# Kernel optimization log

Hardware: AMD Instinct MI355X
Metric: run time of the kernel (lower is better)

## Reference

```python
import jax, jax.numpy as jnp
import numpy as np

# CUBA-LIF constants (from LavaNetwork.__init__ with beta=0.95)
THRESHOLD = 1.0
CURRENT_DECAY = 1.0   # current[t] = (1-1.0)*current[t-1] + input[t] == input[t]
VOLTAGE_DECAY = 1.0 - 0.95  # = 0.05, so v[t] = 0.95*v[t-1] + cur[t]

N_INPUT, N_HIDDEN, N_OUTPUT = 512, 2048, 4 * 64
B, T = 32, 1024


def setup_inputs() -> dict:
    key = jax.random.key(0)
    kx, k1, k2, k3, k4 = jax.random.split(key, 5)
    x = (jax.random.uniform(kx, (B, N_INPUT, T)) < 0.1).astype(jnp.float32)
    # learned params (Linear with bias); small scale so spiking is reasonable
    w1 = jax.random.normal(k1, (N_HIDDEN, N_INPUT), dtype=jnp.float32) * (1.0 / np.sqrt(N_INPUT))
    b1 = jax.random.normal(k2, (N_HIDDEN,), dtype=jnp.float32) * 0.01
    w2 = jax.random.normal(k3, (N_OUTPUT, N_HIDDEN), dtype=jnp.float32) * (1.0 / np.sqrt(N_HIDDEN))
    b2 = jax.random.normal(k4, (N_OUTPUT,), dtype=jnp.float32) * 0.01
    return {"x": x, "w1": w1, "b1": b1, "w2": w2, "b2": b2}


def _cuba_lif(cur):
    """CUBA neuron with current_decay=1 (current==synaptic input),
    leaky-integrate voltage, fire at threshold, reset voltage to 0.
    cur: (B, N, T) -> spikes (B, N, T)."""
    beta_v = 1.0 - VOLTAGE_DECAY  # 0.95

    def step(v, c_t):
        v = v * beta_v + c_t
        s = (v >= THRESHOLD).astype(v.dtype)
        v = v * (1.0 - s)  # reset-to-zero on spike (Loihi behavior)
        return v, s

    cur_t = jnp.moveaxis(cur, -1, 0)  # (T, B, N)
    v0 = jnp.zeros(cur.shape[:-1], cur.dtype)
    _, spk = jax.lax.scan(step, v0, cur_t)
    return jnp.moveaxis(spk, 0, -1)  # (B, N, T)


def reference(x, w1, b1, w2, b2):
    # layer 1: synapse (einsum 'bit,oi->bot' + bias) -> CUBA neuron
    cur1 = jnp.einsum('bit,oi->bot', x, w1) + b1[None, :, None]
    spk1 = _cuba_lif(cur1)
    # layer 2
    cur2 = jnp.einsum('bit,oi->bot', spk1, w2) + b2[None, :, None]
    spk2 = _cuba_lif(cur2)
    return (spk1, spk2)
```

## Files before the change

kernel.cpp:

```cpp
#include <hip/hip_runtime.h>


typedef int i32x4 __attribute__((ext_vector_type(4)));
typedef _Float16 f16x8 __attribute__((ext_vector_type(8)));
typedef _Float16 f16x4 __attribute__((ext_vector_type(4)));
typedef float f32x4 __attribute__((ext_vector_type(4)));

#define GLDS(g, l) __builtin_amdgcn_global_load_lds( \
    (const __attribute__((address_space(1))) void*)(g), \
    (__attribute__((address_space(3))) void*)(l), 16, 0, 0)

#define INV231 4.656612873077392578125e-10


__global__ __launch_bounds__(256) void prep_w8(const float* __restrict__ A,
                                               signed char* __restrict__ wp,
                                               int M, int K)
{
    long gt = (long)blockIdx.x * 256 + threadIdx.x;
    int kq4 = K >> 2;
    int m = (int)(gt / kq4), kq = (int)(gt % kq4);
    int k0 = kq * 4;
    int kt = k0 >> 6, kin = k0 & 63;
    int cw = ((kin >> 4) ^ (m >> 1)) & 3;
    float4 w = *(const float4*)&A[(long)m * K + k0];
    float wv[4] = {w.x, w.y, w.z, w.w};
    int pack[4] = {0, 0, 0, 0};
#pragma unroll
    for (int e = 0; e < 4; e++) {
        long k64 = (long)rint((double)wv[e] * 2147483648.0);
#pragma unroll
        for (int j = 0; j < 3; j++) {
            long r = ((k64 + 128) & 255) - 128;
            pack[j] |= ((int)r & 255) << (e * 8);
            k64 = (k64 - r) >> 8;
        }
        pack[3] |= ((int)k64 & 255) << (e * 8);
    }
#pragma unroll
    for (int p = 0; p < 4; p++)
        *(int*)&wp[(((long)kt * 4 + p) * M + m) * 64 + cw * 16 + (kin & 15)] = pack[p];
}

__global__ __launch_bounds__(256) void prep_x8(const float* __restrict__ x,
                                               unsigned char* __restrict__ xt)
{
    __shared__ float xs[64][68];
    const int b = blockIdx.z, i0 = blockIdx.y * 64, t0 = blockIdx.x * 64;
    const float* xb = x + ((long)b * 512 + i0) * 1024 + t0;
#pragma unroll
    for (int p = 0; p < 4; p++) {
        int f = threadIdx.x + p * 256;
        int i = f >> 4, t4 = (f & 15) * 4;
        *(float4*)&xs[i][t4] = *(const float4*)&xb[(long)i * 1024 + t4];
    }
    __syncthreads();
    int tt = threadIdx.x >> 2, c = threadIdx.x & 3;
    unsigned char bytes[16];
#pragma unroll
    for (int j = 0; j < 16; j++)
        bytes[j] = (unsigned char)xs[c * 16 + j][tt];
    *(uint4*)&xt[(((long)b * 8 + (i0 >> 6)) * 1024 + t0 + tt) * 64 + c * 16] =
        *(uint4*)bytes;
}

__global__ __launch_bounds__(320) void gemm_lif1(
    const signed char* __restrict__ wp,
    const unsigned char* __restrict__ act,
    const float* __restrict__ bias,
    unsigned* __restrict__ mask_ws)
{
    __shared__ signed char Ws[8][4][32][64];
    __shared__ float cs[2][256][33];

    const int b = blockIdx.x, m0 = blockIdx.y * 32;
    const int tid = threadIdx.x, lane = tid & 63, wave = tid >> 6;
    const int lm = lane & 15, lq = lane >> 4;
    const int fro = ((lq ^ (lm >> 1)) & 3) * 16;
    const unsigned char* ab = act + (long)b * 8 * 1024 * 64;

    i32x4 areg[2][4];
    double bv0 = 0.0, bv1 = 0.0;

    if (wave < 4) {
        const int gl_row = lane >> 2, gl_col = (lane & 3) * 16;
#pragma unroll
        for (int j = 0; j < 8; ++j) {
            const int r = wave + 4 * j;
            const int kt = r >> 2, p = r & 3;
            const signed char* g = wp + ((long)r * 2048 + m0 + gl_row) * 64 + gl_col;
            GLDS(g, &Ws[kt][p][0][0]);
            GLDS(g + 16 * 64, &Ws[kt][p][16][0]);
        }
        bv0 = (double)bias[m0 + lm];
        bv1 = (double)bias[m0 + 16 + lm];
#pragma unroll
        for (int f = 0; f < 4; f++)
            areg[0][f] = *(const i32x4*)
                &ab[((long)(wave * 64 + f * 16 + lm)) * 64 + lq * 16];
    }
    __syncthreads();

    double u = 0.0;
    bool sprev = false;

    for (int p = 0; p < 5; ++p) {
        if (wave < 4 && p < 4) {
            i32x4 acc[4][8];
#pragma unroll
            for (int pp = 0; pp < 4; pp++)
#pragma unroll
                for (int q = 0; q < 8; q++) acc[pp][q] = (i32x4)0;

#pragma unroll
            for (int kk = 0; kk < 8; ++kk) {
                {
                    int pn = p, kn = kk + 1;
                    if (kn == 8) { kn = 0; pn = p + 1; if (pn > 3) { pn = 3; kn = 7; } }
                    const long tt = (long)pn * 256 + wave * 64 + lm;
#pragma unroll
                    for (int f = 0; f < 4; f++)
                        areg[(kk + 1) & 1][f] = *(const i32x4*)
                            &ab[((long)kn * 1024 + tt + f * 16) * 64 + lq * 16];
                }
#pragma unroll
                for (int pp = 0; pp < 4; pp++) {
                    i32x4 w0 = *(const i32x4*)&Ws[kk][pp][lm][fro];
                    i32x4 w1 = *(const i32x4*)&Ws[kk][pp][16 + lm][fro];
#pragma unroll
                    for (int f = 0; f < 4; f++) {
                        acc[pp][f * 2 + 0] = __builtin_amdgcn_mfma_i32_16x16x64_i8(
                            areg[kk & 1][f], w0, acc[pp][f * 2 + 0], 0, 0, 0);
                        acc[pp][f * 2 + 1] = __builtin_amdgcn_mfma_i32_16x16x64_i8(
                            areg[kk & 1][f], w1, acc[pp][f * 2 + 1], 0, 0, 0);
                    }
                }
            }
            const int tb = wave * 64;
#pragma unroll
            for (int tf = 0; tf < 4; tf++)
#pragma unroll
                for (int r = 0; r < 4; r++) {
                    const int tl = tb + tf * 16 + lq * 4 + r;
#pragma unroll
                    for (int mf = 0; mf < 2; mf++) {
                        long T = acc[3][tf * 2 + mf][r];
                        T = T * 256 + acc[2][tf * 2 + mf][r];
                        T = T * 256 + acc[1][tf * 2 + mf][r];
                        T = T * 256 + acc[0][tf * 2 + mf][r];
                        cs[p & 1][tl][mf * 16 + lm] =
                            (float)((double)T * INV231 + (mf ? bv1 : bv0));
                    }
                }
        }
        if (wave == 4 && p >= 1 && lane < 32) {
            const int pp = p - 1, buf = pp & 1;
#pragma unroll 1
            for (int g = 0; g < 8; ++g) {
                unsigned mword = 0;
#pragma unroll
                for (int j = 0; j < 32; ++j) {
                    double c = (double)cs[buf][g * 32 + j][lane];
                    double a = 0.95 * u + c;
                    u = sprev ? c : a;
                    bool s = (u >= 1.0);
                    mword |= (s ? 1u : 0u) << j;
                    sprev = s;
                }
                mask_ws[((long)b * 32 + pp * 8 + g) * 2048 + m0 + lane] = mword;
            }
        }
        __syncthreads();
    }
}


__global__ __launch_bounds__(256) void expand_spk8(
    const unsigned* __restrict__ mask_ws,
    unsigned char* __restrict__ spk8)
{
    __shared__ unsigned msk[64][33];
    const int b = blockIdx.x, kt = blockIdx.y;
    const int tid = threadIdx.x;
#pragma unroll
    for (int i = 0; i < 8; ++i) {
        int idx = tid + i * 256;
        int tw = idx >> 6, m = idx & 63;
        msk[m][tw] = mask_ws[((long)b * 32 + tw) * 2048 + kt * 64 + m];
    }
    __syncthreads();
    unsigned char* dst = spk8 + ((long)b * 32 + kt) * 1024 * 64;
#pragma unroll
    for (int i = 0; i < 16; ++i) {
        int off = tid + i * 256;
        int t = off >> 2, mq = off & 3;
        int tw = t >> 5, sh = t & 31;
        unsigned w0 = 0, w1 = 0, w2 = 0, w3 = 0;
#pragma unroll
        for (int j = 0; j < 4; ++j) {
            w0 |= ((msk[mq * 16 + j][tw] >> sh) & 1u) << (8 * j);
            w1 |= ((msk[mq * 16 + 4 + j][tw] >> sh) & 1u) << (8 * j);
            w2 |= ((msk[mq * 16 + 8 + j][tw] >> sh) & 1u) << (8 * j);
            w3 |= ((msk[mq * 16 + 12 + j][tw] >> sh) & 1u) << (8 * j);
        }
        *(uint4*)&dst[(long)off * 16] = (uint4){w0, w1, w2, w3};
    }
}

__global__ __launch_bounds__(256) void expand_spk(
    const unsigned* __restrict__ mask_ws,
    float* __restrict__ spk1)
{
    __shared__ unsigned msk[8][32];
    const long rowbase = (long)blockIdx.x * 8;
    const int b = (int)(rowbase >> 11), m0 = (int)(rowbase & 2047);
    const int tid = threadIdx.x;
    {
        int w = tid >> 3, r = tid & 7;
        msk[r][w] = mask_ws[((long)b * 32 + w) * 2048 + m0 + r];
    }
    __syncthreads();
    const int r = tid >> 5, l5 = tid & 31;
    float* dst = spk1 + (rowbase + r) * 1024;
    const int sh = (l5 & 7) * 4;
#pragma unroll
    for (int j = 0; j < 8; j++) {
        const int t = l5 * 4 + j * 128;
        const unsigned w = msk[r][(l5 >> 3) + j * 4];
        float4 o;
        o.x = ((w >> sh) & 1u) ? 1.f : 0.f;
        o.y = ((w >> (sh + 1)) & 1u) ? 1.f : 0.f;
        o.z = ((w >> (sh + 2)) & 1u) ? 1.f : 0.f;
        o.w = ((w >> (sh + 3)) & 1u) ? 1.f : 0.f;
        *(float4*)&dst[t] = o;
    }
}

template <bool TRANS, int NITER, int CHUNK>
__global__ __launch_bounds__(256, 2) void gemm_i8(
    const signed char* __restrict__ wp,
    const unsigned char* __restrict__ act,
    const float* __restrict__ bias,
    float* __restrict__ C,
    int M)
{
    constexpr int NCHUNK = NITER / CHUNK;
    __shared__ signed char Ws[CHUNK][4][32][64];

    const int b = blockIdx.y;
    const int m0 = blockIdx.z * 32, t0 = blockIdx.x * 256;
    const int tid = threadIdx.x, lane = tid & 63, wave = tid >> 6;
    const int wt = t0 + wave * 64;
    const int lm = lane & 15, lq = lane >> 4;
    const int fro = ((lq ^ (lm >> 1)) & 3) * 16;
    const int gl_row = lane >> 2, gl_col = (lane & 3) * 16;

    const unsigned char* ab = act + (long)b * NITER * 1024 * 64;

    auto stage = [&](int cc) {
#pragma unroll
        for (int j = 0; j < CHUNK; ++j) {
            const int r = wave + 4 * j;
            const int kt = r >> 2, p = r & 3;
            const long kg = ((long)(cc * CHUNK + kt) * 4 + p);
            const signed char* g = wp + (kg * M + m0 + gl_row) * 64 + gl_col;
            GLDS(g, &Ws[kt][p][0][0]);
            GLDS(g + 16 * 64, &Ws[kt][p][16][0]);
        }
    };

    i32x4 acc[4][8];
#pragma unroll
    for (int p = 0; p < 4; p++)
#pragma unroll
        for (int q = 0; q < 8; q++) acc[p][q] = (i32x4)0;

    stage(0);
    i32x4 areg[2][4];
#pragma unroll
    for (int f = 0; f < 4; f++)
        areg[0][f] = *(const i32x4*)&ab[((long)(wt + f * 16 + lm)) * 64 + lq * 16];
    __syncthreads();

    for (int c = 0; c < NCHUNK; ++c) {
#pragma unroll
        for (int kk = 0; kk < CHUNK; ++kk) {
            {
                const int itv = c * CHUNK + kk;
                const long nx = (itv + 1 < NITER) ? itv + 1 : itv;
#pragma unroll
                for (int f = 0; f < 4; f++)
                    areg[(kk + 1) & 1][f] = *(const i32x4*)
                        &ab[(nx * 1024 + wt + f * 16 + lm) * 64 + lq * 16];
            }
#pragma unroll
            for (int p = 0; p < 4; p++) {
                i32x4 w0 = *(const i32x4*)&Ws[kk][p][lm][fro];
                i32x4 w1 = *(const i32x4*)&Ws[kk][p][16 + lm][fro];
                if (TRANS) {
#pragma unroll
                    for (int f = 0; f < 4; f++) {
                        acc[p][f * 2 + 0] = __builtin_amdgcn_mfma_i32_16x16x64_i8(
                            areg[kk & 1][f], w0, acc[p][f * 2 + 0], 0, 0, 0);
                        acc[p][f * 2 + 1] = __builtin_amdgcn_mfma_i32_16x16x64_i8(
                            areg[kk & 1][f], w1, acc[p][f * 2 + 1], 0, 0, 0);
                    }
                } else {
#pragma unroll
                    for (int f = 0; f < 4; f++) {
                        acc[p][0 + f] = __builtin_amdgcn_mfma_i32_16x16x64_i8(
                            w0, areg[kk & 1][f], acc[p][0 + f], 0, 0, 0);
                        acc[p][4 + f] = __builtin_amdgcn_mfma_i32_16x16x64_i8(
                            w1, areg[kk & 1][f], acc[p][4 + f], 0, 0, 0);
                    }
                }
            }
        }
        if (c + 1 < NCHUNK) {
            __syncthreads();
            stage(c + 1);
            __syncthreads();
        }
    }

    if (TRANS) {
        double bv[2];
        bv[0] = (double)bias[m0 + lm];
        bv[1] = (double)bias[m0 + 16 + lm];
        float* Cb = C + (long)b * 1024 * M;
#pragma unroll
        for (int tf = 0; tf < 4; tf++)
#pragma unroll
            for (int r = 0; r < 4; r++) {
                const int trow = wt + tf * 16 + lq * 4 + r;
#pragma unroll
                for (int mf = 0; mf < 2; mf++) {
                    long T = acc[3][tf * 2 + mf][r];
                    T = T * 256 + acc[2][tf * 2 + mf][r];
                    T = T * 256 + acc[1][tf * 2 + mf][r];
                    T = T * 256 + acc[0][tf * 2 + mf][r];
                    Cb[(long)trow * M + m0 + mf * 16 + lm] =
                        (float)((double)T * INV231 + bv[mf]);
                }
            }
    } else {
        float* Cb = C + (long)b * M * 1024;
#pragma unroll
        for (int mf = 0; mf < 2; mf++)
#pragma unroll
            for (int r = 0; r < 4; r++) {
                const int mrow = m0 + mf * 16 + lq * 4 + r;
                const double bv = (double)bias[mrow];
#pragma unroll
                for (int tf = 0; tf < 4; tf++) {
                    long T = acc[3][mf * 4 + tf][r];
                    T = T * 256 + acc[2][mf * 4 + tf][r];
                    T = T * 256 + acc[1][mf * 4 + tf][r];
                    T = T * 256 + acc[0][mf * 4 + tf][r];
                    Cb[(long)mrow * 1024 + wt + tf * 16 + lm] =
                        (float)((double)T * INV231 + bv);
                }
            }
    }
}

template <int RPB>
__global__ __launch_bounds__(256) void lif_lds(float* __restrict__ cur)
{
    __shared__ float cs[RPB][36];
    const long rowbase = (long)blockIdx.x * RPB;
    float* base = cur + rowbase * 1024;
    const int tid = threadIdx.x;
    double v = 0.0;
    const int NV = RPB * 32 / 4;
    for (int tc = 0; tc < 1024; tc += 32) {
        for (int f = tid; f < NV; f += 256) {
            int row = f >> 3, t4 = (f & 7) * 4;
            *(float4*)&cs[row][t4] = *(const float4*)&base[(long)row * 1024 + tc + t4];
        }
        __syncthreads();
        if (tid < RPB) {
#pragma unroll
            for (int j = 0; j < 32; j++) {
                v = 0.95 * v + (double)cs[tid][j];
                bool s = v >= 1.0;
                cs[tid][j] = s ? 1.f : 0.f;
                if (s) v = 0.0;
            }
        }
        __syncthreads();
        for (int f = tid; f < NV; f += 256) {
            int row = f >> 3, t4 = (f & 7) * 4;
            *(float4*)&base[(long)row * 1024 + tc + t4] = *(float4*)&cs[row][t4];
        }
        __syncthreads();
    }
}


__device__ inline void split3(float w, _Float16& q0, _Float16& q1, _Float16& q2) {
    float p0 = rintf(w * 4096.f) * 2.44140625e-4f;
    float r1 = w - p0;
    float p1s = rintf(r1 * 8388608.f) * 2.44140625e-4f;
    float r2 = r1 - p1s * 4.8828125e-4f;
    float p2s = rintf(r2 * 1.7179869184e10f) * 1.220703125e-4f;
    q0 = (_Float16)p0; q1 = (_Float16)p1s; q2 = (_Float16)p2s;
}

__global__ __launch_bounds__(256) void gemm_f16x3_kernel(
    const float* __restrict__ A, const float* __restrict__ Bmat,
    const float* __restrict__ bias, float* __restrict__ C,
    int M, int N, int K, long sB, long sC)
{
    __shared__ _Float16 As[3][128][40];
    __shared__ _Float16 Bsh[128][40];
    const int batch = blockIdx.z;
    const float* Bp = Bmat + (long)batch * sB;
    float* Cp = C + (long)batch * sC;
    const int m0 = blockIdx.y * 128, n0 = blockIdx.x * 128;
    const int tid = threadIdx.x, lane = tid & 63, wave = tid >> 6;
    const int wrow = (wave >> 1) * 64, wcol = (wave & 1) * 64;
    const int lm = lane & 15, lq = lane >> 4;
    const int a_mo = tid >> 3, a_kc = (tid & 7) * 4;
    const int b_kq = tid >> 5, b_nq = tid & 31;

    f32x4 acc[3][4][4];
#pragma unroll
    for (int p = 0; p < 3; p++)
#pragma unroll
        for (int i = 0; i < 4; i++)
#pragma unroll
            for (int j = 0; j < 4; j++) acc[p][i][j] = (f32x4)0.f;

    for (int k0 = 0; k0 < K; k0 += 32) {
#pragma unroll
        for (int i = 0; i < 4; i++) {
            const int m = i * 32 + a_mo;
            float4 w = *(const float4*)&A[(long)(m0 + m) * K + k0 + a_kc];
            _Float16 a0[4], a1[4], a2[4];
            split3(w.x, a0[0], a1[0], a2[0]);
            split3(w.y, a0[1], a1[1], a2[1]);
            split3(w.z, a0[2], a1[2], a2[2]);
            split3(w.w, a0[3], a1[3], a2[3]);
            *(f16x4*)&As[0][m][a_kc] = (f16x4){a0[0], a0[1], a0[2], a0[3]};
            *(f16x4*)&As[1][m][a_kc] = (f16x4){a1[0], a1[1], a1[2], a1[3]};
            *(f16x4*)&As[2][m][a_kc] = (f16x4){a2[0], a2[1], a2[2], a2[3]};
        }
        {
            float4 r0 = *(const float4*)&Bp[(long)(k0 + b_kq * 4 + 0) * N + n0 + b_nq * 4];
            float4 r1 = *(const float4*)&Bp[(long)(k0 + b_kq * 4 + 1) * N + n0 + b_nq * 4];
            float4 r2 = *(const float4*)&Bp[(long)(k0 + b_kq * 4 + 2) * N + n0 + b_nq * 4];
            float4 r3 = *(const float4*)&Bp[(long)(k0 + b_kq * 4 + 3) * N + n0 + b_nq * 4];
            *(f16x4*)&Bsh[b_nq * 4 + 0][b_kq * 4] =
                (f16x4){(_Float16)r0.x, (_Float16)r1.x, (_Float16)r2.x, (_Float16)r3.x};
            *(f16x4*)&Bsh[b_nq * 4 + 1][b_kq * 4] =
                (f16x4){(_Float16)r0.y, (_Float16)r1.y, (_Float16)r2.y, (_Float16)r3.y};
            *(f16x4*)&Bsh[b_nq * 4 + 2][b_kq * 4] =
                (f16x4){(_Float16)r0.z, (_Float16)r1.z, (_Float16)r2.z, (_Float16)r3.z};
            *(f16x4*)&Bsh[b_nq * 4 + 3][b_kq * 4] =
                (f16x4){(_Float16)r0.w, (_Float16)r1.w, (_Float16)r2.w, (_Float16)r3.w};
        }
        __syncthreads();
        f16x8 bf[4];
#pragma unroll
        for (int j = 0; j < 4; j++)
            bf[j] = *(const f16x8*)&Bsh[wcol + j * 16 + lm][lq * 8];
#pragma unroll
        for (int p = 0; p < 3; p++) {
            f16x8 af[4];
#pragma unroll
            for (int i = 0; i < 4; i++)
                af[i] = *(const f16x8*)&As[p][wrow + i * 16 + lm][lq * 8];
#pragma unroll
            for (int i = 0; i < 4; i++)
#pragma unroll
                for (int j = 0; j < 4; j++)
                    acc[p][i][j] = __builtin_amdgcn_mfma_f32_16x16x32_f16(
                        af[i], bf[j], acc[p][i][j], 0, 0, 0);
        }
        __syncthreads();
    }
#pragma unroll
    for (int i = 0; i < 4; i++)
#pragma unroll
        for (int r = 0; r < 4; r++) {
            const int row = m0 + wrow + i * 16 + lq * 4 + r;
            const double bv = (double)bias[row];
#pragma unroll
            for (int j = 0; j < 4; j++) {
                double s = (double)acc[0][i][j][r]
                         + (double)acc[1][i][j][r] * 4.8828125e-4
                         + (double)acc[2][i][j][r] * 4.76837158203125e-7 + bv;
                Cp[(long)row * N + n0 + wcol + j * 16 + lm] = (float)s;
            }
        }
}

__global__ __launch_bounds__(256) void lif_rows(float* __restrict__ data,
                                                long nrows, int T)
{
    long r = (long)blockIdx.x * blockDim.x + threadIdx.x;
    if (r >= nrows) return;
    float* p = data + r * (long)T;
    double v = 0.0;
    for (int t = 0; t < T; t += 4) {
        float4 c = *(float4*)(p + t);
        float4 s;
        v = 0.95 * v + (double)c.x; s.x = (v >= 1.0) ? 1.f : 0.f; if (v >= 1.0) v = 0.0;
        v = 0.95 * v + (double)c.y; s.y = (v >= 1.0) ? 1.f : 0.f; if (v >= 1.0) v = 0.0;
        v = 0.95 * v + (double)c.z; s.z = (v >= 1.0) ? 1.f : 0.f; if (v >= 1.0) v = 0.0;
        v = 0.95 * v + (double)c.w; s.w = (v >= 1.0) ? 1.f : 0.f; if (v >= 1.0) v = 0.0;
        *(float4*)(p + t) = s;
    }
}


extern "C" void kernel_launch(void* const* d_in, const int* in_sizes, int n_in,
                              void* d_out, int out_size, void* d_ws, size_t ws_size,
                              hipStream_t stream)
{
    const float* x  = (const float*)d_in[0];
    const float* w1 = (const float*)d_in[1];
    const float* b1 = (const float*)d_in[2];
    const float* w2 = (const float*)d_in[3];
    const float* b2 = (const float*)d_in[4];

    float* out  = (float*)d_out;
    float* spk1 = out;
    float* spk2 = out + (long)32 * 2048 * 1024;

    const size_t WP1 = 4194304;
    const size_t WP2 = 2097152;
    const size_t X8T = 16777216;
    const size_t SPK = 67108864;
    const size_t MSK = 8388608;
    const size_t NEED = WP1 + WP2 + X8T + SPK + MSK;

    if (ws_size >= NEED) {
        char* ws = (char*)d_ws;
        signed char* wp1 = (signed char*)ws;
        signed char* wp2 = (signed char*)(ws + WP1);
        unsigned char* x8t = (unsigned char*)(ws + WP1 + WP2);
        unsigned char* spk8 = (unsigned char*)(ws + WP1 + WP2 + X8T);
        unsigned* mask_ws = (unsigned*)(ws + WP1 + WP2 + X8T + SPK);

        prep_w8<<<1024, 256, 0, stream>>>(w1, wp1, 2048, 512);
        prep_w8<<<512, 256, 0, stream>>>(w2, wp2, 256, 2048);
        prep_x8<<<dim3(16, 8, 32), 256, 0, stream>>>(x, x8t);

        gemm_lif1<<<dim3(32, 64), 320, 0, stream>>>(wp1, x8t, b1, mask_ws);
        expand_spk8<<<dim3(32, 32), 256, 0, stream>>>(mask_ws, spk8);

        gemm_i8<false, 32, 8><<<dim3(4, 32, 8), 256, 0, stream>>>(
            wp2, spk8, b2, spk2, 256);
        lif_lds<32><<<256, 256, 0, stream>>>(spk2);

        expand_spk<<<8192, 256, 0, stream>>>(mask_ws, spk1);
    } else {
        gemm_f16x3_kernel<<<dim3(8, 16, 32), 256, 0, stream>>>(
            w1, x, b1, spk1, 2048, 1024, 512, (long)512 * 1024, (long)2048 * 1024);
        lif_rows<<<(65536 + 255) / 256, 256, 0, stream>>>(spk1, 65536, 1024);
        gemm_f16x3_kernel<<<dim3(8, 2, 32), 256, 0, stream>>>(
            w2, spk1, b2, spk2, 256, 1024, 2048, (long)2048 * 1024, (long)256 * 1024);
        lif_rows<<<(8192 + 255) / 256, 256, 0, stream>>>(spk2, 8192, 1024);
    }
}
```

Before: 677.4 us.

## Shrink gemm_lif1 tiles to 16 neurons and 128-step phases for more blocks

Reworks the fused layer-1 GEMM+LIF kernel so each block handles 16 output neurons instead of 32, with 2 MFMA waves plus one LIF wave, and processes time in 8 phases of 128 steps instead of 4 of 256. The grid grows from 2048 to 4096 blocks, LDS per block drops, and launch bounds request 2 blocks per SM. The aim is to cut the serial LIF scan latency per phase and raise occupancy, so the scan overlaps better with MFMA work. The costs are more phases and barriers, a weight tile that is reloaded by twice as many blocks, and activations that are now read for half as many neurons per load.

```diff
diff --git a/kernel.cpp b/kernel.cpp
--- a/kernel.cpp
+++ b/kernel.cpp
@@ -64,36 +64,34 @@
         *(uint4*)bytes;
 }
 
-__global__ __launch_bounds__(320) void gemm_lif1(
+__global__ __launch_bounds__(192, 2) void gemm_lif1(
     const signed char* __restrict__ wp,
     const unsigned char* __restrict__ act,
     const float* __restrict__ bias,
     unsigned* __restrict__ mask_ws)
 {
-    __shared__ signed char Ws[8][4][32][64];
-    __shared__ float cs[2][256][33];
-
-    const int b = blockIdx.x, m0 = blockIdx.y * 32;
+    __shared__ signed char Ws[8][4][16][64];
+    __shared__ float cs[2][128][17];
+
+    const int m0 = blockIdx.x * 16, b = blockIdx.y;
     const int tid = threadIdx.x, lane = tid & 63, wave = tid >> 6;
     const int lm = lane & 15, lq = lane >> 4;
     const int fro = ((lq ^ (lm >> 1)) & 3) * 16;
     const unsigned char* ab = act + (long)b * 8 * 1024 * 64;
 
     i32x4 areg[2][4];
-    double bv0 = 0.0, bv1 = 0.0;
-
-    if (wave < 4) {
+    double bv0 = 0.0;
+
+    if (wave < 2) {
         const int gl_row = lane >> 2, gl_col = (lane & 3) * 16;
 #pragma unroll
-        for (int j = 0; j < 8; ++j) {
-            const int r = wave + 4 * j;
+        for (int j = 0; j < 16; ++j) {
+            const int r = wave + 2 * j;
             const int kt = r >> 2, p = r & 3;
             const signed char* g = wp + ((long)r * 2048 + m0 + gl_row) * 64 + gl_col;
             GLDS(g, &Ws[kt][p][0][0]);
-            GLDS(g + 16 * 64, &Ws[kt][p][16][0]);
         }
         bv0 = (double)bias[m0 + lm];
-        bv1 = (double)bias[m0 + 16 + lm];
 #pragma unroll
         for (int f = 0; f < 4; f++)
             areg[0][f] = *(const i32x4*)
@@ -104,20 +102,20 @@
     double u = 0.0;
     bool sprev = false;
 
-    for (int p = 0; p < 5; ++p) {
-        if (wave < 4 && p < 4) {
-            i32x4 acc[4][8];
+    for (int p = 0; p < 9; ++p) {
+        if (wave < 2 && p < 8) {
+            i32x4 acc[4][4];
 #pragma unroll
             for (int pp = 0; pp < 4; pp++)
 #pragma unroll
-                for (int q = 0; q < 8; q++) acc[pp][q] = (i32x4)0;
+                for (int f = 0; f < 4; f++) acc[pp][f] = (i32x4)0;
 
 #pragma unroll
             for (int kk = 0; kk < 8; ++kk) {
                 {
                     int pn = p, kn = kk + 1;
-                    if (kn == 8) { kn = 0; pn = p + 1; if (pn > 3) { pn = 3; kn = 7; } }
-                    const long tt = (long)pn * 256 + wave * 64 + lm;
+                    if (kn == 8) { kn = 0; pn = p + 1; if (pn > 7) { pn = 7; kn = 7; } }
+                    const long tt = (long)pn * 128 + wave * 64 + lm;
 #pragma unroll
                     for (int f = 0; f < 4; f++)
                         areg[(kk + 1) & 1][f] = *(const i32x4*)
@@ -126,14 +124,10 @@
 #pragma unroll
                 for (int pp = 0; pp < 4; pp++) {
                     i32x4 w0 = *(const i32x4*)&Ws[kk][pp][lm][fro];
-                    i32x4 w1 = *(const i32x4*)&Ws[kk][pp][16 + lm][fro];
-#pragma unroll
-                    for (int f = 0; f < 4; f++) {
-                        acc[pp][f * 2 + 0] = __builtin_amdgcn_mfma_i32_16x16x64_i8(
-                            areg[kk & 1][f], w0, acc[pp][f * 2 + 0], 0, 0, 0);
-                        acc[pp][f * 2 + 1] = __builtin_amdgcn_mfma_i32_16x16x64_i8(
-                            areg[kk & 1][f], w1, acc[pp][f * 2 + 1], 0, 0, 0);
-                    }
+#pragma unroll
+                    for (int f = 0; f < 4; f++)
+                        acc[pp][f] = __builtin_amdgcn_mfma_i32_16x16x64_i8(
+                            areg[kk & 1][f], w0, acc[pp][f], 0, 0, 0);
                 }
             }
             const int tb = wave * 64;
@@ -141,22 +135,18 @@
             for (int tf = 0; tf < 4; tf++)
 #pragma unroll
                 for (int r = 0; r < 4; r++) {
-                    const int tl = tb + tf * 16 + lq * 4 + r;
-#pragma unroll
-                    for (int mf = 0; mf < 2; mf++) {
-                        long T = acc[3][tf * 2 + mf][r];
-                        T = T * 256 + acc[2][tf * 2 + mf][r];
-                        T = T * 256 + acc[1][tf * 2 + mf][r];
-                        T = T * 256 + acc[0][tf * 2 + mf][r];
-                        cs[p & 1][tl][mf * 16 + lm] =
-                            (float)((double)T * INV231 + (mf ? bv1 : bv0));
-                    }
-                }
-        }
-        if (wave == 4 && p >= 1 && lane < 32) {
-            const int pp = p - 1, buf = pp & 1;
+                    long T = acc[3][tf][r];
+                    T = T * 256 + acc[2][tf][r];
+                    T = T * 256 + acc[1][tf][r];
+                    T = T * 256 + acc[0][tf][r];
+                    cs[p & 1][tb + tf * 16 + lq * 4 + r][lm] =
+                        (float)((double)T * INV231 + bv0);
+                }
+        }
+        if (wave == 2 && p >= 1 && lane < 16) {
+            const int pq = p - 1, buf = pq & 1;
 #pragma unroll 1
-            for (int g = 0; g < 8; ++g) {
+            for (int g = 0; g < 4; ++g) {
                 unsigned mword = 0;
 #pragma unroll
                 for (int j = 0; j < 32; ++j) {
@@ -167,7 +157,7 @@
                     mword |= (s ? 1u : 0u) << j;
                     sprev = s;
                 }
-                mask_ws[((long)b * 32 + pp * 8 + g) * 2048 + m0 + lane] = mword;
+                mask_ws[((long)b * 32 + pq * 4 + g) * 2048 + m0 + lane] = mword;
             }
         }
         __syncthreads();
@@ -548,7 +538,7 @@
         prep_w8<<<512, 256, 0, stream>>>(w2, wp2, 256, 2048);
         prep_x8<<<dim3(16, 8, 32), 256, 0, stream>>>(x, x8t);
 
-        gemm_lif1<<<dim3(32, 64), 320, 0, stream>>>(wp1, x8t, b1, mask_ws);
+        gemm_lif1<<<dim3(128, 32), 192, 0, stream>>>(wp1, x8t, b1, mask_ws);
         expand_spk8<<<dim3(32, 32), 256, 0, stream>>>(mask_ws, spk8);
 
         gemm_i8<false, 32, 8><<<dim3(4, 32, 8), 256, 0, stream>>>(
```

Result: faster. 658.9 us (-2.7%).
